# Kernel tuning notes

Hardware: AMD Instinct MI355X
Metric: run time of the kernel (lower is better)

Reference implementation:

```python
import jax, jax.numpy as jnp
import numpy as np

N_NODES = 50000
N_EDGES = 800000
IN_DIM = 128
HID_DIM = 128
NUM_GRAPHS = 64


def gcn_conv(x, edge_index, W, b):
    """PyG GCNConv: symmetric-normalized aggregation with self-loops.
    out = D^{-1/2} (A + I) D^{-1/2} (x @ W) + b
    """
    n = x.shape[0]
    loop = jnp.arange(n, dtype=edge_index.dtype)
    src = jnp.concatenate([edge_index[0], loop])  # [E+N]
    dst = jnp.concatenate([edge_index[1], loop])
    deg = jax.ops.segment_sum(jnp.ones_like(dst, x.dtype), dst, num_segments=n)
    dinv = jnp.where(deg > 0, jax.lax.rsqrt(deg), 0.0)
    norm = dinv[src] * dinv[dst]  # [E+N]
    h = x @ W  # [N, H] transform before propagate (PyG order)
    msg = h[src] * norm[:, None]  # [E+N, H] gathered+scaled messages
    out = jax.ops.segment_sum(msg, dst, num_segments=n)  # scatter-add
    return out + b


def global_mean_pool(x, batch, num_graphs):
    s = jax.ops.segment_sum(x, batch, num_segments=num_graphs)
    cnt = jax.ops.segment_sum(jnp.ones((x.shape[0],), x.dtype), batch, num_segments=num_graphs)
    return s / jnp.maximum(cnt, 1.0)[:, None]


def setup_inputs() -> dict:
    key = jax.random.key(0)
    ks = jax.random.split(key, 8)
    x = jax.random.normal(ks[0], (N_NODES, IN_DIM), dtype=jnp.float32)
    edge_index = jax.random.randint(ks[1], (2, N_EDGES), 0, N_NODES, dtype=jnp.int64)
    batch = jnp.sort(jax.random.randint(ks[2], (N_NODES,), 0, NUM_GRAPHS, dtype=jnp.int64))
    s1 = 1.0 / np.sqrt(IN_DIM)
    s2 = 1.0 / np.sqrt(HID_DIM)
    W1 = jax.random.uniform(ks[3], (IN_DIM, HID_DIM), jnp.float32, -s1, s1)
    b1 = jnp.zeros((HID_DIM,), jnp.float32)
    W2 = jax.random.uniform(ks[4], (HID_DIM, HID_DIM), jnp.float32, -s2, s2)
    b2 = jnp.zeros((HID_DIM,), jnp.float32)
    Wc = jax.random.uniform(ks[5], (HID_DIM, 1), jnp.float32, -s2, s2)
    bc = jnp.zeros((1,), jnp.float32)
    return {"x": x, "edge_index": edge_index, "batch": batch,
            "W1": W1, "b1": b1, "W2": W2, "b2": b2, "Wc": Wc, "bc": bc}


def reference(x, edge_index, batch, W1, b1, W2, b2, Wc, bc):
    h = jax.nn.relu(gcn_conv(x, edge_index, W1, b1))
    # dropout p=0.1 is identity in eval mode
    h = gcn_conv(h, edge_index, W2, b2)
    g = global_mean_pool(h, batch, NUM_GRAPHS)  # [G, H]
    return jax.nn.sigmoid(g @ Wc + bc)  # [G, 1]
```

## Files before the change

kernel.cpp:

```cpp
#include <hip/hip_runtime.h>
#include <hip/hip_bf16.h>
#include <hip/hip_fp16.h>

#define N_NODES 50000
#define N_EDGES 800000
#define DIM     128
#define NG      64
#define GN      16
#define CAP     48
#define AGG_EB  256
#define LAXP    136

#define NBIN    196
#define SORT_B  250
#define EPB     3200

#define CAST_B  1563
#define VB_B    129
#define WF_B    8

typedef float  f2_t  __attribute__((ext_vector_type(2)));
typedef float  f32x4 __attribute__((ext_vector_type(4)));
typedef _Float16 f16x8 __attribute__((ext_vector_type(8)));
typedef _Float16 f16x4 __attribute__((ext_vector_type(4)));

__global__ void k_prep(const int* __restrict__ ei, int* __restrict__ binCnt,
                       const float4* __restrict__ x4, uint4* __restrict__ xq4,
                       const float* __restrict__ W2, const float* __restrict__ Wc,
                       const float* __restrict__ b2, float* __restrict__ v,
                       float* __restrict__ beta2,
                       const float* __restrict__ W1, f16x8* __restrict__ w1f) {
    __shared__ float red[4];
    __shared__ int hist[256];
    int bid = blockIdx.x, t = threadIdx.x;
    if (bid < SORT_B) {
        hist[t] = 0;
        __syncthreads();
        int base = bid * EPB;
        for (int r = 0; r < 13; r++) {
            int idx = r * 256 + t;
            if (idx < EPB) {
                int d = ei[N_EDGES + base + idx];
                atomicAdd(&hist[d >> 8], 1);
            }
        }
        __syncthreads();
        if (t < NBIN && hist[t] > 0) atomicAdd(&binCnt[t], hist[t]);
    } else if (bid < SORT_B + CAST_B) {
        int idx = (bid - SORT_B) * 256 + t;
        if (idx < N_NODES * DIM / 16) {
            uint4 o;
            unsigned* op = (unsigned*)&o;
            #pragma unroll
            for (int q = 0; q < 4; q++) {
                float4 f = x4[idx * 4 + q];
                int p = 0;
                p = __builtin_amdgcn_cvt_pk_fp8_f32(f.x, f.y, p, false);
                p = __builtin_amdgcn_cvt_pk_fp8_f32(f.z, f.w, p, true);
                op[q] = (unsigned)p;
            }
            xq4[idx] = o;
        }
    } else if (bid < SORT_B + CAST_B + VB_B) {
        int b = bid - (SORT_B + CAST_B);
        float p = 0.f;
        if (t < DIM) p = (b < DIM) ? W2[b * DIM + t] * Wc[t] : b2[t] * Wc[t];
        #pragma unroll
        for (int off = 32; off > 0; off >>= 1) p += __shfl_down(p, off, 64);
        if ((t & 63) == 0) red[t >> 6] = p;
        __syncthreads();
        if (t == 0) {
            float s = red[0] + red[1];
            if (b < DIM) v[b] = s; else beta2[0] = s;
        }
    } else {
        int idx = (bid - (SORT_B + CAST_B + VB_B)) * 256 + t;
        int ntile = idx >> 8, kb = (idx >> 6) & 3, l = idx & 63;
        int kbase = kb * 32 + (l >> 4) * 8;
        int n = ntile * 16 + (l & 15);
        f16x8 o;
        #pragma unroll
        for (int j = 0; j < 8; j++) o[j] = (_Float16)W1[(kbase + j) * DIM + n];
        w1f[idx] = o;
    }
}

__global__ void k_scatter(const int* __restrict__ ei, const int* __restrict__ binCnt,
                          int* __restrict__ binCur, int* __restrict__ binOff,
                          unsigned int* __restrict__ sorted) {
    __shared__ int soff[256];
    __shared__ int hist[256];
    __shared__ int cur[256];
    int bid = blockIdx.x, t = threadIdx.x;
    int c = (t < NBIN) ? binCnt[t] : 0;
    soff[t] = c;
    #pragma unroll
    for (int o = 1; o < 256; o <<= 1) {
        __syncthreads();
        int v2 = (t >= o) ? soff[t - o] : 0;
        __syncthreads();
        soff[t] += v2;
    }
    __syncthreads();
    int excl = soff[t] - c;
    if (bid == 0 && t < NBIN) binOff[t] = excl;
    hist[t] = 0;
    __syncthreads();
    int base = bid * EPB;
    for (int r = 0; r < 13; r++) {
        int idx = r * 256 + t;
        if (idx < EPB) {
            int d = ei[N_EDGES + base + idx];
            atomicAdd(&hist[d >> 8], 1);
        }
    }
    __syncthreads();
    if (t < NBIN && hist[t] > 0) cur[t] = excl + atomicAdd(&binCur[t], hist[t]);
    __syncthreads();
    for (int r = 0; r < 13; r++) {
        int idx = r * 256 + t;
        if (idx < EPB) {
            int e = base + idx;
            int s = ei[e];
            int d = ei[N_EDGES + e];
            int pos = atomicAdd(&cur[d >> 8], 1);
            sorted[pos] = (unsigned)s | ((unsigned)(d & 255) << 16);
        }
    }
}

__global__ void k_deg(const unsigned int* __restrict__ sorted,
                      const int* __restrict__ binOff, int* __restrict__ deg) {
    __shared__ int cnt[256];
    int b = blockIdx.x, t = threadIdx.x;
    cnt[t] = 0;
    __syncthreads();
    int lo = binOff[b];
    int hi = (b == NBIN - 1) ? N_EDGES : binOff[b + 1];
    for (int i = lo + t; i < hi; i += 256)
        atomicAdd(&cnt[sorted[i] >> 16], 1);
    __syncthreads();
    int node = b * 256 + t;
    if (node < N_NODES) deg[node] = cnt[t];
}

__global__ void k_build(const unsigned int* __restrict__ sorted,
                        const int* __restrict__ binOff, const int* __restrict__ deg,
                        unsigned int* __restrict__ csr) {
    __shared__ int cur[256];
    int b = blockIdx.x, t = threadIdx.x;
    cur[t] = 0;
    __syncthreads();
    int lo = binOff[b];
    int hi = (b == NBIN - 1) ? N_EDGES : binOff[b + 1];
    for (int i = lo + t; i < hi; i += 256) {
        unsigned e = sorted[i];
        unsigned src = e & 0xFFFFu;
        unsigned dLow = e >> 16;
        int pos = atomicAdd(&cur[dLow], 1);
        if (pos < CAP) {
            float w = rsqrtf((float)deg[src] + 1.f);
            unsigned hw = (unsigned)__half_as_ushort(__float2half(w));
            csr[(b * 256 + dLow) * CAP + pos] = src | (hw << 16);
        }
    }
}

__global__ __launch_bounds__(512) void k_node(
    const unsigned int* __restrict__ xq,
    const unsigned int* __restrict__ csr,
    const f16x8* __restrict__ w1f,
    const float* __restrict__ b1,
    const float* __restrict__ v, const int* __restrict__ deg,
    float* __restrict__ z2) {
    __shared__ _Float16 laxh[GN * LAXP];
    __shared__ float redm[GN * 8];
    int tid = threadIdx.x;
    int w = tid >> 6, l = tid & 63;
    int half = l >> 5, hl = l & 31;
    int node0 = blockIdx.x * GN;

    {
        int i = node0 + 2 * w + half;
        int len = min(deg[i], CAP);
        float di = rsqrtf((float)deg[i] + 1.f);

        unsigned su = xq[(size_t)i * 32 + hl];
        f2_t s01 = __builtin_amdgcn_cvt_pk_f32_fp8((int)su, false);
        f2_t s23 = __builtin_amdgcn_cvt_pk_f32_fp8((int)su, true);
        float ax[8], ay[8], az[8], aw[8];
        #pragma unroll
        for (int k = 0; k < 8; k++) { ax[k] = 0.f; ay[k] = 0.f; az[k] = 0.f; aw[k] = 0.f; }
        ax[0] = di * s01.x; ay[0] = di * s01.y;
        az[0] = di * s23.x; aw[0] = di * s23.y;

        int lenmax = max(len, __shfl_xor(len, 32, 64));
        int lmp = (lenmax + 7) & ~7;
        const uint4* csr4 = (const uint4*)csr;
        int base4 = i * (CAP / 4);
        for (int j = 0; j < lmp; j += 8) {
            uint4 ca = csr4[base4 + (j >> 2)];
            uint4 cb = csr4[base4 + (j >> 2) + 1];
            unsigned pe[8] = {ca.x, ca.y, ca.z, ca.w, cb.x, cb.y, cb.z, cb.w};
            unsigned q[8];
            #pragma unroll
            for (int k = 0; k < 8; k++)
                q[k] = xq[(size_t)(pe[k] & 0xFFFFu) * 32 + hl];
            float wgt[8];
            #pragma unroll
            for (int k = 0; k < 8; k++)
                wgt[k] = (j + k < len)
                    ? __half2float(__ushort_as_half((unsigned short)(pe[k] >> 16))) : 0.f;
            #pragma unroll
            for (int k = 0; k < 8; k++) {
                f2_t e01 = __builtin_amdgcn_cvt_pk_f32_fp8((int)q[k], false);
                f2_t e23 = __builtin_amdgcn_cvt_pk_f32_fp8((int)q[k], true);
                ax[k] = fmaf(wgt[k], e01.x, ax[k]);
                ay[k] = fmaf(wgt[k], e01.y, ay[k]);
                az[k] = fmaf(wgt[k], e23.x, az[k]);
                aw[k] = fmaf(wgt[k], e23.y, aw[k]);
            }
        }
        float a0 = 0.f, a1 = 0.f, a2 = 0.f, a3 = 0.f;
        #pragma unroll
        for (int k = 0; k < 8; k++) { a0 += ax[k]; a1 += ay[k]; a2 += az[k]; a3 += aw[k]; }
        f16x4 pk;
        pk[0] = (_Float16)(di * a0); pk[1] = (_Float16)(di * a1);
        pk[2] = (_Float16)(di * a2); pk[3] = (_Float16)(di * a3);
        *(f16x4*)&laxh[(2 * w + half) * LAXP + 4 * hl] = pk;
    }
    __syncthreads();

    f32x4 acc = {0.f, 0.f, 0.f, 0.f};
    #pragma unroll
    for (int kb = 0; kb < 4; kb++) {
        f16x8 af = *(const f16x8*)&laxh[(l & 15) * LAXP + kb * 32 + (l >> 4) * 8];
        f16x8 bf = w1f[(w * 4 + kb) * 64 + l];
        acc = __builtin_amdgcn_mfma_f32_16x16x32_f16(af, bf, acc, 0, 0, 0);
    }
    int n = w * 16 + (l & 15);
    float bn = b1[n], vn = v[n];
    #pragma unroll
    for (int r = 0; r < 4; r++) {
        float p = fmaxf(acc[r] + bn, 0.f) * vn;
        p += __shfl_xor(p, 1, 64);
        p += __shfl_xor(p, 2, 64);
        p += __shfl_xor(p, 4, 64);
        p += __shfl_xor(p, 8, 64);
        if ((l & 15) == 0) redm[((l >> 4) * 4 + r) * 8 + w] = p;
    }
    __syncthreads();
    if (tid < GN) {
        float s = 0.f;
        #pragma unroll
        for (int q = 0; q < 8; q++) s += redm[tid * 8 + q];
        z2[node0 + tid] = rsqrtf((float)deg[node0 + tid] + 1.f) * s;
    }
}

__global__ void k_aggz(const float* __restrict__ z2, const int* __restrict__ deg,
                       const int* __restrict__ ei, const int* __restrict__ batch,
                       float* __restrict__ gpartE, float* __restrict__ gpartN,
                       int* __restrict__ gcnt) {
    int bid = blockIdx.x, t = threadIdx.x;
    if (bid < AGG_EB) {
        __shared__ float bs[4][NG];
        bs[t >> 6][t & 63] = 0.f;
        __syncthreads();
        int wg = t >> 6;
        for (int base = bid * 1024; base < N_EDGES; base += AGG_EB * 1024) {
            #pragma unroll
            for (int k = 0; k < 4; k++) {
                int e = base + k * 256 + t;
                if (e < N_EDGES) {
                    int s = ei[e];
                    int d = ei[N_EDGES + e];
                    float dv = rsqrtf((float)deg[d] + 1.f);
                    atomicAdd(&bs[wg][batch[d]], dv * z2[s]);
                }
            }
        }
        __syncthreads();
        if (t < NG) gpartE[bid * NG + t] = bs[0][t] + bs[1][t] + bs[2][t] + bs[3][t];
    } else {
        __shared__ int range[2];
        __shared__ float rs[4];
        int g = bid - AGG_EB;
        if (t < 2) {
            int key = g + t;
            int lo = 0, hi = N_NODES;
            while (lo < hi) { int m = (lo + hi) >> 1; if (batch[m] < key) lo = m + 1; else hi = m; }
            range[t] = lo;
        }
        __syncthreads();
        int lo = range[0], hi = range[1];
        float loc = 0.f;
        for (int i = lo + t; i < hi; i += 256)
            loc += rsqrtf((float)deg[i] + 1.f) * z2[i];
        #pragma unroll
        for (int off = 32; off > 0; off >>= 1) loc += __shfl_down(loc, off, 64);
        if ((t & 63) == 0) rs[t >> 6] = loc;
        __syncthreads();
        if (t == 0) {
            gpartN[g] = rs[0] + rs[1] + rs[2] + rs[3];
            gcnt[g] = hi - lo;
        }
    }
}

__global__ void k_final(const float* __restrict__ gpartE, const float* __restrict__ gpartN,
                        const int* __restrict__ gcnt, const float* __restrict__ beta2,
                        const float* __restrict__ bcin, float* __restrict__ out) {
    __shared__ float acc[4][NG];
    int t = threadIdx.x;
    int g = t & 63, c = t >> 6;
    float s = 0.f;
    for (int k = 0; k < AGG_EB / 4; k++)
        s += gpartE[(c * (AGG_EB / 4) + k) * NG + g];
    acc[c][g] = s;
    __syncthreads();
    if (t < NG) {
        float tot = acc[0][t] + acc[1][t] + acc[2][t] + acc[3][t] + gpartN[t];
        int cnt = gcnt[t];
        float val = tot / (float)(cnt > 0 ? cnt : 1) + beta2[0] + bcin[0];
        out[t] = 1.f / (1.f + expf(-val));
    }
}

extern "C" void kernel_launch(void* const* d_in, const int* in_sizes, int n_in,
                              void* d_out, int out_size, void* d_ws, size_t ws_size,
                              hipStream_t stream) {
    const float* x   = (const float*)d_in[0];
    const int*   ei  = (const int*)  d_in[1];
    const int*   bat = (const int*)  d_in[2];
    const float* W1  = (const float*)d_in[3];
    const float* b1  = (const float*)d_in[4];
    const float* W2  = (const float*)d_in[5];
    const float* b2  = (const float*)d_in[6];
    const float* Wc  = (const float*)d_in[7];
    const float* bc  = (const float*)d_in[8];
    float* out = (float*)d_out;

    char* w = (char*)d_ws;
    size_t off = 0;
    auto alloc = [&](size_t bytes) -> void* {
        void* p = w + off;
        off = (off + bytes + 255) & ~(size_t)255;
        return p;
    };
    int*   binCnt  = (int*)  alloc(NBIN * 4);
    int*   binCur  = (int*)  alloc(NBIN * 4);
    size_t zero_len = off;
    int*   binOff  = (int*)  alloc(NBIN * 4);
    int*   deg     = (int*)  alloc(N_NODES * 4);
    float* z2      = (float*)alloc(N_NODES * 4);
    float* v       = (float*)alloc(DIM * 4);
    float* beta2   = (float*)alloc(4);
    float* gpartE  = (float*)alloc((size_t)AGG_EB * NG * 4);
    float* gpartN  = (float*)alloc(NG * 4);
    int*   gcnt    = (int*)  alloc(NG * 4);
    f16x8* w1f     = (f16x8*)alloc(2048 * 16);
    unsigned int* xq     = (unsigned int*)alloc((size_t)N_NODES * DIM);
    unsigned int* sorted = (unsigned int*)alloc((size_t)N_EDGES * 4);
    unsigned int* csr    = (unsigned int*)alloc((size_t)N_NODES * CAP * 4);
    (void)ws_size; (void)in_sizes; (void)n_in; (void)out_size;

    hipMemsetAsync(d_ws, 0, zero_len, stream);

    dim3 b256(256);
    k_prep<<<dim3(SORT_B + CAST_B + VB_B + WF_B), b256, 0, stream>>>(
        ei, binCnt, (const float4*)x, (uint4*)xq, W2, Wc, b2, v, beta2, W1, w1f);
    k_scatter<<<dim3(SORT_B), b256, 0, stream>>>(ei, binCnt, binCur, binOff, sorted);
    k_deg<<<dim3(NBIN), b256, 0, stream>>>(sorted, binOff, deg);
    k_build<<<dim3(NBIN), b256, 0, stream>>>(sorted, binOff, deg, csr);
    k_node<<<dim3(N_NODES / GN), dim3(512), 0, stream>>>(
        xq, csr, w1f, b1, v, deg, z2);
    k_aggz<<<dim3(AGG_EB + NG), b256, 0, stream>>>(z2, deg, ei, bat, gpartE, gpartN, gcnt);
    k_final<<<dim3(1), b256, 0, stream>>>(gpartE, gpartN, gcnt, beta2, bc, out);
}
```

Before: 167.8 us.

## Process 64 nodes per block with 8 lanes per node and 16-byte gathers

The node kernel now handles 64 nodes per block instead of 16. Each node's neighbour aggregation is done by 8 lanes that each load a 16-byte FP8 chunk, replacing 32 lanes that each loaded 4 bytes. The MFMA stage is reorganised so each wave computes 4 output tiles over a 16-row slice, and the partial dot products are accumulated in registers before one reduction. The goal is fewer, wider gather transactions and better amortisation of the weight fragments and block overhead. In exchange each lane holds more registers, neighbour lists are walked two at a time with per-lane clamping, and a bounds check is needed for the last partial block.

```diff
diff --git a/kernel.cpp b/kernel.cpp
--- a/kernel.cpp
+++ b/kernel.cpp
@@ -6,10 +6,10 @@
 #define N_EDGES 800000
 #define DIM     128
 #define NG      64
-#define GN      16
 #define CAP     48
 #define AGG_EB  256
 #define LAXP    136
+#define NODE_B  782
 
 #define NBIN    196
 #define SORT_B  250
@@ -22,7 +22,19 @@
 typedef float  f2_t  __attribute__((ext_vector_type(2)));
 typedef float  f32x4 __attribute__((ext_vector_type(4)));
 typedef _Float16 f16x8 __attribute__((ext_vector_type(8)));
-typedef _Float16 f16x4 __attribute__((ext_vector_type(4)));
+
+__device__ __forceinline__ void fma16(float* acc, float wgt, uint4 q) {
+    unsigned u[4] = {q.x, q.y, q.z, q.w};
+    #pragma unroll
+    for (int c = 0; c < 4; c++) {
+        f2_t lo = __builtin_amdgcn_cvt_pk_f32_fp8((int)u[c], false);
+        f2_t hi = __builtin_amdgcn_cvt_pk_f32_fp8((int)u[c], true);
+        acc[4 * c + 0] = fmaf(wgt, lo.x, acc[4 * c + 0]);
+        acc[4 * c + 1] = fmaf(wgt, lo.y, acc[4 * c + 1]);
+        acc[4 * c + 2] = fmaf(wgt, hi.x, acc[4 * c + 2]);
+        acc[4 * c + 3] = fmaf(wgt, hi.y, acc[4 * c + 3]);
+    }
+}
 
 __global__ void k_prep(const int* __restrict__ ei, int* __restrict__ binCnt,
                        const float4* __restrict__ x4, uint4* __restrict__ xq4,
@@ -167,94 +179,98 @@
 }
 
 __global__ __launch_bounds__(512) void k_node(
-    const unsigned int* __restrict__ xq,
+    const uint4* __restrict__ xq4,
     const unsigned int* __restrict__ csr,
     const f16x8* __restrict__ w1f,
     const float* __restrict__ b1,
     const float* __restrict__ v, const int* __restrict__ deg,
     float* __restrict__ z2) {
-    __shared__ _Float16 laxh[GN * LAXP];
-    __shared__ float redm[GN * 8];
+    __shared__ _Float16 laxh[64 * LAXP];
+    __shared__ float redm[64 * 2];
     int tid = threadIdx.x;
     int w = tid >> 6, l = tid & 63;
-    int half = l >> 5, hl = l & 31;
-    int node0 = blockIdx.x * GN;
+    int og = l >> 3, ol = l & 7;
+    int node0 = blockIdx.x * 64;
 
     {
-        int i = node0 + 2 * w + half;
-        int len = min(deg[i], CAP);
-        float di = rsqrtf((float)deg[i] + 1.f);
-
-        unsigned su = xq[(size_t)i * 32 + hl];
-        f2_t s01 = __builtin_amdgcn_cvt_pk_f32_fp8((int)su, false);
-        f2_t s23 = __builtin_amdgcn_cvt_pk_f32_fp8((int)su, true);
-        float ax[8], ay[8], az[8], aw[8];
-        #pragma unroll
-        for (int k = 0; k < 8; k++) { ax[k] = 0.f; ay[k] = 0.f; az[k] = 0.f; aw[k] = 0.f; }
-        ax[0] = di * s01.x; ay[0] = di * s01.y;
-        az[0] = di * s23.x; aw[0] = di * s23.y;
-
-        int lenmax = max(len, __shfl_xor(len, 32, 64));
-        int lmp = (lenmax + 7) & ~7;
-        const uint4* csr4 = (const uint4*)csr;
-        int base4 = i * (CAP / 4);
-        for (int j = 0; j < lmp; j += 8) {
-            uint4 ca = csr4[base4 + (j >> 2)];
-            uint4 cb = csr4[base4 + (j >> 2) + 1];
-            unsigned pe[8] = {ca.x, ca.y, ca.z, ca.w, cb.x, cb.y, cb.z, cb.w};
-            unsigned q[8];
-            #pragma unroll
-            for (int k = 0; k < 8; k++)
-                q[k] = xq[(size_t)(pe[k] & 0xFFFFu) * 32 + hl];
-            float wgt[8];
-            #pragma unroll
-            for (int k = 0; k < 8; k++)
-                wgt[k] = (j + k < len)
-                    ? __half2float(__ushort_as_half((unsigned short)(pe[k] >> 16))) : 0.f;
-            #pragma unroll
-            for (int k = 0; k < 8; k++) {
-                f2_t e01 = __builtin_amdgcn_cvt_pk_f32_fp8((int)q[k], false);
-                f2_t e23 = __builtin_amdgcn_cvt_pk_f32_fp8((int)q[k], true);
-                ax[k] = fmaf(wgt[k], e01.x, ax[k]);
-                ay[k] = fmaf(wgt[k], e01.y, ay[k]);
-                az[k] = fmaf(wgt[k], e23.x, az[k]);
-                aw[k] = fmaf(wgt[k], e23.y, aw[k]);
-            }
-        }
-        float a0 = 0.f, a1 = 0.f, a2 = 0.f, a3 = 0.f;
-        #pragma unroll
-        for (int k = 0; k < 8; k++) { a0 += ax[k]; a1 += ay[k]; a2 += az[k]; a3 += aw[k]; }
-        f16x4 pk;
-        pk[0] = (_Float16)(di * a0); pk[1] = (_Float16)(di * a1);
-        pk[2] = (_Float16)(di * a2); pk[3] = (_Float16)(di * a3);
-        *(f16x4*)&laxh[(2 * w + half) * LAXP + 4 * hl] = pk;
-    }
-    __syncthreads();
-
-    f32x4 acc = {0.f, 0.f, 0.f, 0.f};
-    #pragma unroll
-    for (int kb = 0; kb < 4; kb++) {
-        f16x8 af = *(const f16x8*)&laxh[(l & 15) * LAXP + kb * 32 + (l >> 4) * 8];
-        f16x8 bf = w1f[(w * 4 + kb) * 64 + l];
-        acc = __builtin_amdgcn_mfma_f32_16x16x32_f16(af, bf, acc, 0, 0, 0);
-    }
-    int n = w * 16 + (l & 15);
-    float bn = b1[n], vn = v[n];
-    #pragma unroll
-    for (int r = 0; r < 4; r++) {
-        float p = fmaxf(acc[r] + bn, 0.f) * vn;
-        p += __shfl_xor(p, 1, 64);
-        p += __shfl_xor(p, 2, 64);
-        p += __shfl_xor(p, 4, 64);
-        p += __shfl_xor(p, 8, 64);
-        if ((l & 15) == 0) redm[((l >> 4) * 4 + r) * 8 + w] = p;
-    }
-    __syncthreads();
-    if (tid < GN) {
-        float s = 0.f;
-        #pragma unroll
-        for (int q = 0; q < 8; q++) s += redm[tid * 8 + q];
-        z2[node0 + tid] = rsqrtf((float)deg[node0 + tid] + 1.f) * s;
+        int i = node0 + 8 * w + og;
+        bool valid = (i < N_NODES);
+        int ic = valid ? i : 0;
+        int len = valid ? min(deg[ic], CAP) : 0;
+        int start = ic * CAP;
+        int lm1 = (len > 0) ? len - 1 : 0;
+        float di = rsqrtf((float)deg[ic] + 1.f);
+
+        float acc[16];
+        #pragma unroll
+        for (int k = 0; k < 16; k++) acc[k] = 0.f;
+        fma16(acc, di, xq4[(size_t)ic * 8 + ol]);
+
+        int lenmax = len;
+        lenmax = max(lenmax, __shfl_xor(lenmax, 8, 64));
+        lenmax = max(lenmax, __shfl_xor(lenmax, 16, 64));
+        lenmax = max(lenmax, __shfl_xor(lenmax, 32, 64));
+
+        for (int j = 0; j < lenmax; j += 2) {
+            int j0 = min(j, lm1), j1 = min(j + 1, lm1);
+            unsigned e0 = csr[start + j0];
+            unsigned e1 = csr[start + j1];
+            float w0 = (j < len) ? __half2float(__ushort_as_half((unsigned short)(e0 >> 16))) : 0.f;
+            float w1 = (j + 1 < len) ? __half2float(__ushort_as_half((unsigned short)(e1 >> 16))) : 0.f;
+            uint4 r0 = xq4[(size_t)(e0 & 0xFFFFu) * 8 + ol];
+            uint4 r1 = xq4[(size_t)(e1 & 0xFFFFu) * 8 + ol];
+            fma16(acc, w0, r0);
+            fma16(acc, w1, r1);
+        }
+        int row = 8 * w + og;
+        f16x8 lo, hi;
+        #pragma unroll
+        for (int k = 0; k < 8; k++) {
+            lo[k] = (_Float16)(di * acc[k]);
+            hi[k] = (_Float16)(di * acc[8 + k]);
+        }
+        *(f16x8*)&laxh[row * LAXP + 16 * ol] = lo;
+        *(f16x8*)&laxh[row * LAXP + 16 * ol + 8] = hi;
+    }
+    __syncthreads();
+
+    {
+        int m = w & 3, nh = w >> 2;
+        float rs[4] = {0.f, 0.f, 0.f, 0.f};
+        #pragma unroll
+        for (int c = 0; c < 4; c++) {
+            int nt = nh * 4 + c;
+            f32x4 accv = {0.f, 0.f, 0.f, 0.f};
+            #pragma unroll
+            for (int kb = 0; kb < 4; kb++) {
+                f16x8 af = *(const f16x8*)&laxh[(16 * m + (l & 15)) * LAXP + kb * 32 + (l >> 4) * 8];
+                f16x8 bf = w1f[(nt * 4 + kb) * 64 + l];
+                accv = __builtin_amdgcn_mfma_f32_16x16x32_f16(af, bf, accv, 0, 0, 0);
+            }
+            int n = nt * 16 + (l & 15);
+            float bn = b1[n], vn = v[n];
+            #pragma unroll
+            for (int r = 0; r < 4; r++) {
+                float p = fmaxf(accv[r] + bn, 0.f) * vn;
+                p += __shfl_xor(p, 1, 64);
+                p += __shfl_xor(p, 2, 64);
+                p += __shfl_xor(p, 4, 64);
+                p += __shfl_xor(p, 8, 64);
+                rs[r] += p;
+            }
+        }
+        if ((l & 15) == 0) {
+            int q = l >> 4;
+            #pragma unroll
+            for (int r = 0; r < 4; r++)
+                redm[(16 * m + q * 4 + r) * 2 + nh] = rs[r];
+        }
+    }
+    __syncthreads();
+    if (tid < 64) {
+        int node = node0 + tid;
+        if (node < N_NODES)
+            z2[node] = rsqrtf((float)deg[node] + 1.f) * (redm[tid * 2] + redm[tid * 2 + 1]);
     }
 }
 
@@ -373,8 +389,8 @@
     k_scatter<<<dim3(SORT_B), b256, 0, stream>>>(ei, binCnt, binCur, binOff, sorted);
     k_deg<<<dim3(NBIN), b256, 0, stream>>>(sorted, binOff, deg);
     k_build<<<dim3(NBIN), b256, 0, stream>>>(sorted, binOff, deg, csr);
-    k_node<<<dim3(N_NODES / GN), dim3(512), 0, stream>>>(
-        xq, csr, w1f, b1, v, deg, z2);
+    k_node<<<dim3(NODE_B), dim3(512), 0, stream>>>(
+        (const uint4*)xq, csr, w1f, b1, v, deg, z2);
     k_aggz<<<dim3(AGG_EB + NG), b256, 0, stream>>>(z2, deg, ei, bat, gpartE, gpartN, gcnt);
     k_final<<<dim3(1), b256, 0, stream>>>(gpartE, gpartN, gcnt, beta2, bc, out);
 }
```

Result: slower. 173.3 us (+3.3%).

## Aggregate z2 over dst-binned sorted edges and fuse final reduction via last-block

Applied to the files above, without the earlier changes.

The final per-graph aggregation now walks the already dst-binned sorted edge list, one block per 256-node bin. Each block caches the batch id and degree scale of its destination nodes in shared memory instead of gathering them per edge from global memory. Node self-terms and graph counts are computed in the same pass. The separate final kernel is replaced by a last-block-done pattern using an atomic counter, which saves one launch. The cost is fewer blocks (196) and a serial 196-way reduction in the last block. Graphs with zero nodes now output sigmoid(bc), where the old code output sigmoid(beta2+bc).

```diff
diff --git a/kernel.cpp b/kernel.cpp
--- a/kernel.cpp
+++ b/kernel.cpp
@@ -8,7 +8,6 @@
 #define NG      64
 #define GN      16
 #define CAP     48
-#define AGG_EB  256
 #define LAXP    136
 
 #define NBIN    196
@@ -259,71 +258,58 @@
 }
 
 __global__ void k_aggz(const float* __restrict__ z2, const int* __restrict__ deg,
-                       const int* __restrict__ ei, const int* __restrict__ batch,
-                       float* __restrict__ gpartE, float* __restrict__ gpartN,
-                       int* __restrict__ gcnt) {
-    int bid = blockIdx.x, t = threadIdx.x;
-    if (bid < AGG_EB) {
-        __shared__ float bs[4][NG];
-        bs[t >> 6][t & 63] = 0.f;
-        __syncthreads();
-        int wg = t >> 6;
-        for (int base = bid * 1024; base < N_EDGES; base += AGG_EB * 1024) {
-            #pragma unroll
-            for (int k = 0; k < 4; k++) {
-                int e = base + k * 256 + t;
-                if (e < N_EDGES) {
-                    int s = ei[e];
-                    int d = ei[N_EDGES + e];
-                    float dv = rsqrtf((float)deg[d] + 1.f);
-                    atomicAdd(&bs[wg][batch[d]], dv * z2[s]);
-                }
+                       const int* __restrict__ batch,
+                       const unsigned int* __restrict__ sorted,
+                       const int* __restrict__ binOff,
+                       float* __restrict__ gpartE, float* __restrict__ gpartC,
+                       int* __restrict__ done,
+                       const float* __restrict__ beta2, const float* __restrict__ bcin,
+                       float* __restrict__ out) {
+    __shared__ float bs[NG];
+    __shared__ float bc[NG];
+    __shared__ int   batL[256];
+    __shared__ float dvL[256];
+    __shared__ int   lastFlag;
+    int b = blockIdx.x, t = threadIdx.x;
+    if (t < NG) { bs[t] = 0.f; bc[t] = 0.f; }
+    int node = b * 256 + t;
+    bool valid = (node < N_NODES);
+    batL[t] = valid ? batch[node] : 0;
+    dvL[t]  = valid ? rsqrtf((float)deg[node] + 1.f) : 0.f;
+    __syncthreads();
+    if (valid) {
+        atomicAdd(&bs[batL[t]], dvL[t] * z2[node]);
+        atomicAdd(&bc[batL[t]], 1.f);
+    }
+    int lo = binOff[b];
+    int hi = (b == NBIN - 1) ? N_EDGES : binOff[b + 1];
+    for (int i = lo + t; i < hi; i += 256) {
+        unsigned e = sorted[i];
+        unsigned src = e & 0xFFFFu;
+        unsigned dLow = e >> 16;
+        atomicAdd(&bs[batL[dLow]], dvL[dLow] * z2[src]);
+    }
+    __syncthreads();
+    if (t < NG) {
+        gpartE[b * NG + t] = bs[t];
+        gpartC[b * NG + t] = bc[t];
+    }
+    if (t == 0) {
+        __threadfence();
+        lastFlag = (atomicAdd(done, 1) == NBIN - 1) ? 1 : 0;
+    }
+    __syncthreads();
+    if (lastFlag) {
+        __threadfence();
+        if (t < NG) {
+            float s = 0.f, c = 0.f;
+            for (int k = 0; k < NBIN; k++) {
+                s += gpartE[k * NG + t];
+                c += gpartC[k * NG + t];
             }
-        }
-        __syncthreads();
-        if (t < NG) gpartE[bid * NG + t] = bs[0][t] + bs[1][t] + bs[2][t] + bs[3][t];
-    } else {
-        __shared__ int range[2];
-        __shared__ float rs[4];
-        int g = bid - AGG_EB;
-        if (t < 2) {
-            int key = g + t;
-            int lo = 0, hi = N_NODES;
-            while (lo < hi) { int m = (lo + hi) >> 1; if (batch[m] < key) lo = m + 1; else hi = m; }
-            range[t] = lo;
-        }
-        __syncthreads();
-        int lo = range[0], hi = range[1];
-        float loc = 0.f;
-        for (int i = lo + t; i < hi; i += 256)
-            loc += rsqrtf((float)deg[i] + 1.f) * z2[i];
-        #pragma unroll
-        for (int off = 32; off > 0; off >>= 1) loc += __shfl_down(loc, off, 64);
-        if ((t & 63) == 0) rs[t >> 6] = loc;
-        __syncthreads();
-        if (t == 0) {
-            gpartN[g] = rs[0] + rs[1] + rs[2] + rs[3];
-            gcnt[g] = hi - lo;
-        }
-    }
-}
-
-__global__ void k_final(const float* __restrict__ gpartE, const float* __restrict__ gpartN,
-                        const int* __restrict__ gcnt, const float* __restrict__ beta2,
-                        const float* __restrict__ bcin, float* __restrict__ out) {
-    __shared__ float acc[4][NG];
-    int t = threadIdx.x;
-    int g = t & 63, c = t >> 6;
-    float s = 0.f;
-    for (int k = 0; k < AGG_EB / 4; k++)
-        s += gpartE[(c * (AGG_EB / 4) + k) * NG + g];
-    acc[c][g] = s;
-    __syncthreads();
-    if (t < NG) {
-        float tot = acc[0][t] + acc[1][t] + acc[2][t] + acc[3][t] + gpartN[t];
-        int cnt = gcnt[t];
-        float val = tot / (float)(cnt > 0 ? cnt : 1) + beta2[0] + bcin[0];
-        out[t] = 1.f / (1.f + expf(-val));
+            float val = (c > 0.5f) ? (s / c + beta2[0] + bcin[0]) : bcin[0];
+            out[t] = 1.f / (1.f + expf(-val));
+        }
     }
 }
 
@@ -350,15 +336,15 @@
     };
     int*   binCnt  = (int*)  alloc(NBIN * 4);
     int*   binCur  = (int*)  alloc(NBIN * 4);
+    int*   done    = (int*)  alloc(4);
     size_t zero_len = off;
     int*   binOff  = (int*)  alloc(NBIN * 4);
     int*   deg     = (int*)  alloc(N_NODES * 4);
     float* z2      = (float*)alloc(N_NODES * 4);
     float* v       = (float*)alloc(DIM * 4);
     float* beta2   = (float*)alloc(4);
-    float* gpartE  = (float*)alloc((size_t)AGG_EB * NG * 4);
-    float* gpartN  = (float*)alloc(NG * 4);
-    int*   gcnt    = (int*)  alloc(NG * 4);
+    float* gpartE  = (float*)alloc((size_t)NBIN * NG * 4);
+    float* gpartC  = (float*)alloc((size_t)NBIN * NG * 4);
     f16x8* w1f     = (f16x8*)alloc(2048 * 16);
     unsigned int* xq     = (unsigned int*)alloc((size_t)N_NODES * DIM);
     unsigned int* sorted = (unsigned int*)alloc((size_t)N_EDGES * 4);
@@ -375,6 +361,6 @@
     k_build<<<dim3(NBIN), b256, 0, stream>>>(sorted, binOff, deg, csr);
     k_node<<<dim3(N_NODES / GN), dim3(512), 0, stream>>>(
         xq, csr, w1f, b1, v, deg, z2);
-    k_aggz<<<dim3(AGG_EB + NG), b256, 0, stream>>>(z2, deg, ei, bat, gpartE, gpartN, gcnt);
-    k_final<<<dim3(1), b256, 0, stream>>>(gpartE, gpartN, gcnt, beta2, bc, out);
-}
+    k_aggz<<<dim3(NBIN), b256, 0, stream>>>(
+        z2, deg, bat, sorted, binOff, gpartE, gpartC, done, beta2, bc, out);
+}
```

Result: slower. 172.5 us (+2.8%).
